# Performance work log

Hardware: AMD Instinct MI355X
Metric: run time of the kernel (lower is better)

The kernel has to match this reference:

```python
import jax, jax.numpy as jnp
import numpy as np


def setup_inputs() -> dict:
    key = jax.random.key(0)
    k1, k2 = jax.random.split(key)
    x = jax.random.normal(k1, (16, 256, 4096), dtype=jnp.float32)          # [B, D, T]
    codebooks = jax.random.normal(k2, (8, 1024, 256), dtype=jnp.float32)   # [n_q, bins, D]
    return {"x": x, "codebooks": codebooks}


def _quantize_one(residual, embed):
    """residual: [B, T, D]; embed: [bins, D] -> (quantize [B,T,D], idx [B,T])."""
    # negative squared euclidean distance (encodec euclidean codebook)
    x_sq = jnp.sum(residual * residual, axis=-1, keepdims=True)            # [B, T, 1]
    e_sq = jnp.sum(embed * embed, axis=-1)                                  # [bins]
    dots = jnp.einsum("btd,nd->btn", residual, embed)                       # [B, T, bins]
    dist = -(x_sq - 2.0 * dots + e_sq)                                      # [B, T, bins]
    idx = jnp.argmax(dist, axis=-1)                                         # [B, T] int
    quantize = embed[idx]                                                   # gather [B, T, D]
    return quantize, idx


def reference(x, codebooks):
    """Residual VQ forward (inference path, EMA updates omitted).
    x: [B, D, T]; codebooks: [n_q, bins, D].
    Returns (quantized [B, D, T], codes [n_q, B, T]).
    """
    n_q = codebooks.shape[0]
    residual = jnp.transpose(x, (0, 2, 1))                                  # [B, T, D]
    quantized_out = jnp.zeros_like(residual)
    codes = []
    for q in range(n_q):  # small fixed structural loop over quantizer stages
        quantize, idx = _quantize_one(residual, codebooks[q])
        # straight-through estimator as in encodec VectorQuantization
        quantize = residual + jax.lax.stop_gradient(quantize - residual)
        residual = residual - quantize
        quantized_out = quantized_out + quantize
        codes.append(idx)
    quantized = jnp.transpose(quantized_out, (0, 2, 1))                     # [B, D, T]
    codes = jnp.stack(codes, axis=0)                                        # [n_q, B, T]
    return quantized, codes
```

## Files before the change

### kernel.cpp

```cpp
#include <hip/hip_runtime.h>


#define BB   16
#define DD   256
#define TT   4096
#define NQ   8
#define BINS 1024
#define DELTA 4.0f
#define SOFF  8192.0f
#define OUTQ ((size_t)BB * DD * TT)

typedef _Float16 half8 __attribute__((ext_vector_type(8)));
typedef float    facc  __attribute__((ext_vector_type(4)));

#define MFMA16(A, B, C) __builtin_amdgcn_mfma_f32_16x16x32_f16((A), (B), (C), 0, 0, 0)

__global__ __launch_bounds__(256)
void rvq_pack_h16(const float* __restrict__ cb, _Float16* __restrict__ pks) {
    int gid = blockIdx.x * 256 + threadIdx.x;
    int s   = gid & 7;
    int bin = (gid >> 3) & 1023;
    int q   = gid >> 13;
    const float* src = cb + ((size_t)(q * BINS + bin)) * DD + s * 32;
    int cc    = q * 32 + (bin >> 5);
    int nf    = (bin >> 4) & 1;
    int c     = bin & 15;
    int plane = nf * 8 + s;
    size_t base = (size_t)cc * 8192 + (size_t)plane * 512 + c * 8;
    #pragma unroll
    for (int g = 0; g < 4; ++g) {
        float4 v0 = *(const float4*)(src + g * 8);
        float4 v1 = *(const float4*)(src + g * 8 + 4);
        float vv[8] = { v0.x, v0.y, v0.z, v0.w, v1.x, v1.y, v1.z, v1.w };
        half8 h8;
        #pragma unroll
        for (int j = 0; j < 8; ++j) h8[j] = (_Float16)vv[j];
        *(half8*)&pks[base + g * 128] = h8;
    }
}

__global__ __launch_bounds__(256)
void rvq_esq_off(const float* __restrict__ cb, float* __restrict__ hoff) {
    int q = blockIdx.x;
    const float* e = cb + (size_t)q * BINS * DD;
    for (int bin = threadIdx.x; bin < BINS; bin += 256) {
        const float4* row = (const float4*)(e + (size_t)bin * DD);
        float s = 0.f;
        #pragma unroll 8
        for (int i = 0; i < DD / 4; ++i) {
            float4 v = row[i];
            s += v.x * v.x + v.y * v.y + v.z * v.z + v.w * v.w;
        }
        hoff[q * BINS + bin] = SOFF - 8.0f * s;
    }
}

__global__ __launch_bounds__(256, 2)
void rvq_mfma6_kernel(const float* __restrict__ x, const float* __restrict__ cb,
                      const _Float16* __restrict__ pks, const float* __restrict__ hoff,
                      float* __restrict__ out)
{
    __shared__ alignas(16) _Float16 btile[2][16][512];
    __shared__ unsigned short best_lds[4][32];
    __shared__ unsigned short hist_lds[4][NQ][32];

    const int tid = threadIdx.x;
    const int w   = tid >> 6;
    const int l   = tid & 63;
    const int c   = l & 15;
    const int g   = l >> 4;

    const int blk = blockIdx.x;
    const int b   = blk >> 5;
    const int t0  = (blk & 31) * 128;
    const int tw  = t0 + w * 32;

    const char* gsrc0 = (const char*)pks + w * 4096 + (l << 4);

    auto issue_chunk = [&](int k, int bu) {
        k &= 255;
        const char* src = gsrc0 + (size_t)k * 16384;
        char* dst = (char*)(&btile[bu][0][0]) + w * 4096;
        #pragma unroll
        for (int i = 0; i < 4; ++i) {
            __builtin_amdgcn_global_load_lds(
                (const __attribute__((address_space(1))) unsigned int*)(src + i * 1024),
                (__attribute__((address_space(3))) unsigned int*)(dst + i * 1024),
                16, 0, 0);
        }
    };

    issue_chunk(0, 0);

    half8 rh[2][8], rl[2][8];
    {
        const float* xb = x + (size_t)b * DD * TT;
        #pragma unroll
        for (int s = 0; s < 8; ++s) {
            #pragma unroll
            for (int j = 0; j < 8; ++j) {
                int d = s * 32 + g * 8 + j;
                #pragma unroll
                for (int m = 0; m < 2; ++m) {
                    int t = tw + m * 16 + c;
                    float v = 16.0f * xb[(size_t)d * TT + t];
                    _Float16 h = (_Float16)v;
                    rh[m][s][j] = h;
                    rl[m][s][j] = (_Float16)(v - (float)h);
                }
            }
        }
    }
    __syncthreads();

    float p1[2][4], p2[2][4], p3[2][4];

    auto reset_slots = [&]() {
        #pragma unroll
        for (int m = 0; m < 2; ++m)
            #pragma unroll
            for (int j = 0; j < 4; ++j) { p1[m][j] = 0.f; p2[m][j] = 0.f; p3[m][j] = 0.f; }
    };

    auto compute_chunk = [&](int bu, int qq, int ch) {
        facc a00 = {0.f,0.f,0.f,0.f}, a01 = {0.f,0.f,0.f,0.f};
        facc a10 = {0.f,0.f,0.f,0.f}, a11 = {0.f,0.f,0.f,0.f};
        const int roff = g * 128 + c * 8;
        const float* hq = hoff + qq * BINS + ch * 32;
        float q0 = hq[c], q1 = hq[16 + c];
        const _Float16 (*bt)[512] = btile[bu];

        __builtin_amdgcn_s_setprio(1);
        #pragma unroll
        for (int s = 0; s < 8; ++s) {
            half8 b0 = *(const half8*)&bt[s][roff];
            half8 b1 = *(const half8*)&bt[8 + s][roff];
            a00 = MFMA16(rh[0][s], b0, a00);
            a10 = MFMA16(rh[1][s], b0, a10);
            a01 = MFMA16(rh[0][s], b1, a01);
            a11 = MFMA16(rh[1][s], b1, a11);
        }
        __builtin_amdgcn_s_setprio(0);

        const unsigned idx0 = 1023u - (unsigned)(ch * 32 + c);
        const unsigned idx1 = idx0 - 16u;
        #pragma unroll
        for (int fm = 0; fm < 2; ++fm) {
            #pragma unroll
            for (int fj = 0; fj < 4; ++fj) {
                float s0 = (fm ? a10[fj] : a00[fj]) + q0;
                float s1 = (fm ? a11[fj] : a01[fj]) + q1;
                float v0 = __builtin_bit_cast(float,
                             (__builtin_bit_cast(unsigned, s0) & ~1023u) | idx0);
                float v1 = __builtin_bit_cast(float,
                             (__builtin_bit_cast(unsigned, s1) & ~1023u) | idx1);
                float h1 = fmaxf(p1[fm][fj], v0), l1 = fminf(p1[fm][fj], v0);
                float h2 = fmaxf(p2[fm][fj], l1), l2 = fminf(p2[fm][fj], l1);
                p1[fm][fj] = h1; p2[fm][fj] = h2; p3[fm][fj] = fmaxf(p3[fm][fj], l2);
                h1 = fmaxf(p1[fm][fj], v1); l1 = fminf(p1[fm][fj], v1);
                h2 = fmaxf(p2[fm][fj], l1); l2 = fminf(p2[fm][fj], l1);
                p1[fm][fj] = h1; p2[fm][fj] = h2; p3[fm][fj] = fmaxf(p3[fm][fj], l2);
            }
        }
    };

    auto refine3 = [&](int tkl, int qq, int c1, int c2, int c3) -> int {
        int t = tw + tkl;
        double pa = 0.0, pb = 0.0, pc = 0.0;
        const float* e1p = cb + (size_t)(qq * BINS + c1) * DD;
        const float* e2p = cb + (size_t)(qq * BINS + c2) * DD;
        const float* e3p = cb + (size_t)(qq * BINS + c3) * DD;
        #pragma unroll
        for (int dd = 0; dd < 4; ++dd) {
            int d = l * 4 + dd;
            float rv = x[((size_t)b * DD + d) * TT + t];
            for (int k = 0; k < qq; ++k) {
                int hb = hist_lds[w][k][tkl];
                rv -= cb[(size_t)(k * BINS + hb) * DD + d];
            }
            float e1v = e1p[d], e2v = e2p[d], e3v = e3p[d];
            pa += (double)e1v * (2.0 * (double)rv - (double)e1v);
            pb += (double)e2v * (2.0 * (double)rv - (double)e2v);
            pc += (double)e3v * (2.0 * (double)rv - (double)e3v);
        }
        #pragma unroll
        for (int mk = 1; mk < 64; mk <<= 1) {
            pa += __shfl_xor(pa, mk);
            pb += __shfl_xor(pb, mk);
            pc += __shfl_xor(pc, mk);
        }
        int wbin = c1; double pw = pa;
        if (pb > pw || (pb == pw && c2 < wbin)) { pw = pb; wbin = c2; }
        if (pc > pw || (pc == pw && c3 < wbin)) { pw = pc; wbin = c3; }
        return wbin;
    };

    auto stage_end = [&](int qq) {
        int  bch[2][4], cn2[2][4], cn3[2][4];
        bool gate[2][4];
        #pragma unroll
        for (int fm = 0; fm < 2; ++fm) {
            #pragma unroll
            for (int fj = 0; fj < 4; ++fj) {
                float a1 = p1[fm][fj], a2 = p2[fm][fj], a3 = p3[fm][fj];
                #pragma unroll
                for (int mk = 1; mk < 16; mk <<= 1) {
                    float b1 = __shfl_xor(a1, mk);
                    float b2 = __shfl_xor(a2, mk);
                    float b3 = __shfl_xor(a3, mk);
                    float lo1 = fminf(a1, b1);
                    float m22 = fmaxf(a2, b2);
                    float r1  = fmaxf(a1, b1);
                    float r2  = fmaxf(lo1, m22);
                    float r3  = fmaxf(fminf(lo1, m22), fmaxf(fminf(a2, b2), fmaxf(a3, b3)));
                    a1 = r1; a2 = r2; a3 = r3;
                }
                bch[fm][fj] = 1023 - (int)(__builtin_bit_cast(unsigned, a1) & 1023u);
                cn2[fm][fj] = 1023 - (int)(__builtin_bit_cast(unsigned, a2) & 1023u);
                cn3[fm][fj] = 1023 - (int)(__builtin_bit_cast(unsigned, a3) & 1023u);
                gate[fm][fj] = (a1 - a2 <= DELTA);
            }
        }
        bool anyg = gate[0][0] | gate[0][1] | gate[0][2] | gate[0][3]
                  | gate[1][0] | gate[1][1] | gate[1][2] | gate[1][3];
        if (__any(anyg)) {
            #pragma unroll
            for (int fm = 0; fm < 2; ++fm) {
                #pragma unroll
                for (int fj = 0; fj < 4; ++fj) {
                    unsigned long long nm = __ballot(gate[fm][fj]);
                    if (nm) {
                        for (int g2 = 0; g2 < 4; ++g2) {
                            if ((nm >> (g2 * 16)) & 1ull) {
                                int c1 = __shfl(bch[fm][fj], g2 * 16);
                                int c2 = __shfl(cn2[fm][fj], g2 * 16);
                                int c3 = __shfl(cn3[fm][fj], g2 * 16);
                                int tkl = fm * 16 + g2 * 4 + fj;
                                int wb = refine3(tkl, qq, c1, c2, c3);
                                if (g == g2) bch[fm][fj] = wb;
                            }
                        }
                    }
                }
            }
        }

        if (c == 0) {
            #pragma unroll
            for (int fm = 0; fm < 2; ++fm)
                #pragma unroll
                for (int fj = 0; fj < 4; ++fj) {
                    int tkl = fm * 16 + g * 4 + fj;
                    best_lds[w][tkl] = (unsigned short)bch[fm][fj];
                    hist_lds[w][qq][tkl] = (unsigned short)bch[fm][fj];
                    out[OUTQ + ((size_t)qq * BB + b) * TT + tw + tkl] = (float)bch[fm][fj];
                }
        }

        #pragma unroll
        for (int m = 0; m < 2; ++m) {
            int bin = best_lds[w][m * 16 + c];
            const float* ep = cb + (size_t)(qq * BINS + bin) * DD + g * 8;
            #pragma unroll
            for (int s = 0; s < 8; ++s) {
                float4 e0 = *(const float4*)(ep + s * 32);
                float4 e1 = *(const float4*)(ep + s * 32 + 4);
                float ev[8] = { e0.x, e0.y, e0.z, e0.w, e1.x, e1.y, e1.z, e1.w };
                #pragma unroll
                for (int j = 0; j < 8; ++j) {
                    float rv = (float)rh[m][s][j] + (float)rl[m][s][j];
                    float nr = rv - 16.0f * ev[j];
                    _Float16 nh = (_Float16)nr;
                    rh[m][s][j] = nh;
                    rl[m][s][j] = (_Float16)(nr - (float)nh);
                }
            }
        }
    };

    int buf = 0;
    for (int q = 0; q < NQ; ++q) {
        reset_slots();
        for (int ch = 0; ch < 32; ++ch) {
            issue_chunk(q * 32 + ch + 1, buf ^ 1);
            compute_chunk(buf, q, ch);
            if (ch == 31) stage_end(q);
            __syncthreads();
            buf ^= 1;
        }
    }

    {
        const float* xb = x + (size_t)b * DD * TT;
        float* ob = out + (size_t)b * DD * TT;
        #pragma unroll
        for (int s = 0; s < 8; ++s)
            #pragma unroll
            for (int j = 0; j < 8; ++j) {
                int d = s * 32 + g * 8 + j;
                #pragma unroll
                for (int m = 0; m < 2; ++m) {
                    int t = tw + m * 16 + c;
                    float rv = ((float)rh[m][s][j] + (float)rl[m][s][j]) * 0.0625f;
                    ob[(size_t)d * TT + t] = xb[(size_t)d * TT + t] - rv;
                }
            }
    }
}

#define TOK_PER_BLK 32
#define BIN_CHUNK   128
#define KC          32
#define EPAD        36
#define RPAD        260
#define FDELTA      0.0078125f

#define FUPD2(S, BIN, B1, I1, B2, I2)                                        \
    if ((S) > (B2) || ((S) == (B2) && (BIN) < (I2))) {                      \
        if ((S) > (B1) || ((S) == (B1) && (BIN) < (I1))) {                  \
            B2 = B1; I2 = I1; B1 = (S); I1 = (BIN);                         \
        } else { B2 = (S); I2 = (BIN); }                                    \
    }

__global__ __launch_bounds__(256, 2)
void rvq_esq_kernel(const float* __restrict__ cb, float* __restrict__ esq) {
    int q = blockIdx.x;
    const float* e = cb + (size_t)q * BINS * DD;
    for (int bin = threadIdx.x; bin < BINS; bin += 256) {
        const float4* row = (const float4*)(e + (size_t)bin * DD);
        float s = 0.f;
        #pragma unroll 8
        for (int i = 0; i < DD / 4; ++i) {
            float4 v = row[i];
            s += v.x * v.x + v.y * v.y + v.z * v.z + v.w * v.w;
        }
        esq[q * BINS + bin] = s;
    }
}

__global__ __launch_bounds__(256, 2)
void rvq_main_kernel(const float* __restrict__ x, const float* __restrict__ cb,
                     const float* __restrict__ esq, float* __restrict__ out) {
    __shared__ float r_lds[TOK_PER_BLK][RPAD];
    __shared__ float e_lds[BIN_CHUNK][EPAD];
    __shared__ float red_s[16][2][TOK_PER_BLK];
    __shared__ int   red_i[16][2][TOK_PER_BLK];
    __shared__ int   best_lds2[TOK_PER_BLK];

    const int tid = threadIdx.x;
    const int blk = blockIdx.x;
    const int b   = blk >> 7;
    const int t0  = (blk & 127) * TOK_PER_BLK;

    {
        const int tl = tid & 31;
        const int d0 = (tid >> 5) * 32;
        const float* xp = x + (size_t)b * DD * TT + t0 + tl;
        for (int dd = 0; dd < 32; ++dd) {
            int d = d0 + dd;
            r_lds[tl][d] = xp[(size_t)d * TT];
        }
    }
    __syncthreads();

    const int ty = tid >> 4;
    const int tx = tid & 15;

    for (int q = 0; q < NQ; ++q) {
        const float* eb = cb + (size_t)q * BINS * DD;
        const float* es = esq + q * BINS;
        float b1[2] = {-1e30f, -1e30f}, b2[2] = {-1e30f, -1e30f};
        int   i1[2] = {0x7fffffff, 0x7fffffff}, i2[2] = {0x7fffffff, 0x7fffffff};

        for (int cch = 0; cch < BINS / BIN_CHUNK; ++cch) {
            float acc[2][8];
            #pragma unroll
            for (int i = 0; i < 2; ++i)
                #pragma unroll
                for (int j = 0; j < 8; ++j) acc[i][j] = 0.f;

            for (int kc = 0; kc < DD / KC; ++kc) {
                __syncthreads();
                {
                    const int col  = tid & 7;
                    const int row0 = tid >> 3;
                    const float* src = eb + (size_t)(cch * BIN_CHUNK) * DD + kc * KC;
                    #pragma unroll
                    for (int rr = 0; rr < 4; ++rr) {
                        int row = row0 + rr * 32;
                        float4 v = *(const float4*)(src + (size_t)row * DD + col * 4);
                        *(float4*)&e_lds[row][col * 4] = v;
                    }
                }
                __syncthreads();
                #pragma unroll
                for (int k4 = 0; k4 < KC / 4; ++k4) {
                    float4 r0 = *(const float4*)&r_lds[tx][kc * KC + k4 * 4];
                    float4 r1 = *(const float4*)&r_lds[tx + 16][kc * KC + k4 * 4];
                    #pragma unroll
                    for (int bi = 0; bi < 8; ++bi) {
                        float4 e4 = *(const float4*)&e_lds[ty + 16 * bi][k4 * 4];
                        acc[0][bi] += r0.x * e4.x + r0.y * e4.y + r0.z * e4.z + r0.w * e4.w;
                        acc[1][bi] += r1.x * e4.x + r1.y * e4.y + r1.z * e4.z + r1.w * e4.w;
                    }
                }
            }
            #pragma unroll
            for (int bi = 0; bi < 8; ++bi) {
                int bin = cch * BIN_CHUNK + ty + 16 * bi;
                float half_esq = 0.5f * es[bin];
                float s0 = acc[0][bi] - half_esq;
                float s1v = acc[1][bi] - half_esq;
                FUPD2(s0, bin, b1[0], i1[0], b2[0], i2[0]);
                FUPD2(s1v, bin, b1[1], i1[1], b2[1], i2[1]);
            }
        }

        #pragma unroll
        for (int k = 0; k < 2; ++k) {
            red_s[ty][k][tx]      = k ? b2[0] : b1[0];
            red_i[ty][k][tx]      = k ? i2[0] : i1[0];
            red_s[ty][k][tx + 16] = k ? b2[1] : b1[1];
            red_i[ty][k][tx + 16] = k ? i2[1] : i1[1];
        }
        __syncthreads();

        if (tid < TOK_PER_BLK) {
            float g1 = -1e30f, g2 = -1e30f; int gi1 = 0x7fffffff, gi2 = 0x7fffffff;
            #pragma unroll
            for (int j = 0; j < 16; ++j) {
                #pragma unroll
                for (int k = 0; k < 2; ++k) {
                    float s = red_s[j][k][tid]; int ii = red_i[j][k][tid];
                    FUPD2(s, ii, g1, gi1, g2, gi2);
                }
            }
            int bif;
            if (g1 - g2 <= FDELTA) {
                const float* rrow = r_lds[tid];
                double sc[2]; int id2[2] = { gi1, gi2 };
                for (int cc2 = 0; cc2 < 2; ++cc2) {
                    const float* ep = eb + (size_t)id2[cc2] * DD;
                    double acc2 = 0.0;
                    #pragma unroll 4
                    for (int d = 0; d < DD; ++d) {
                        double ev = (double)ep[d];
                        acc2 += ev * (2.0 * (double)rrow[d] - ev);
                    }
                    sc[cc2] = acc2;
                }
                bif = (sc[0] > sc[1] || (sc[0] == sc[1] && id2[0] < id2[1])) ? id2[0] : id2[1];
            } else {
                bif = gi1;
            }
            best_lds2[tid] = bif;
            out[OUTQ + (size_t)q * (BB * TT) + (size_t)b * TT + t0 + tid] = (float)bif;
        }
        __syncthreads();

        {
            const int tok  = tid >> 3;
            const int part = tid & 7;
            const int bin  = best_lds2[tok];
            const float* ep = eb + (size_t)bin * DD + part * 32;
            float* rp = &r_lds[tok][part * 32];
            #pragma unroll
            for (int dd = 0; dd < 32; ++dd) rp[dd] -= ep[dd];
        }
        __syncthreads();
    }

    {
        const int tl = tid & 31;
        const int d0 = (tid >> 5) * 32;
        const float* xp = x + (size_t)b * DD * TT + t0 + tl;
        float*       op = out + (size_t)b * DD * TT + t0 + tl;
        for (int dd = 0; dd < 32; ++dd) {
            int d = d0 + dd;
            op[(size_t)d * TT] = xp[(size_t)d * TT] - r_lds[tl][d];
        }
    }
}

extern "C" void kernel_launch(void* const* d_in, const int* in_sizes, int n_in,
                              void* d_out, int out_size, void* d_ws, size_t ws_size,
                              hipStream_t stream) {
    const float* x  = (const float*)d_in[0];
    const float* cb = (const float*)d_in[1];
    float* out = (float*)d_out;

    const size_t PKS_BYTES = (size_t)NQ * BINS * DD * 2;
    const size_t NEED = PKS_BYTES + (size_t)NQ * BINS * 4;

    if (ws_size >= NEED) {
        _Float16* pks = (_Float16*)d_ws;
        float* hoff = (float*)((char*)d_ws + PKS_BYTES);
        rvq_pack_h16<<<(NQ * BINS * 8) / 256, 256, 0, stream>>>(cb, pks);
        rvq_esq_off<<<NQ, 256, 0, stream>>>(cb, hoff);
        rvq_mfma6_kernel<<<512, 256, 0, stream>>>(x, cb, pks, hoff, out);
    } else {
        float* esq = (float*)d_ws;
        rvq_esq_kernel<<<NQ, 256, 0, stream>>>(cb, esq);
        rvq_main_kernel<<<(BB * TT) / TOK_PER_BLK, 256, 0, stream>>>(x, cb, esq, out);
    }
}
```

Before: 652.9 us.

## Double chunk staging to pairs per barrier and stage codebook norms in LDS

The main loop now loads two 32-bin codebook chunks per pipeline step, halving the number of __syncthreads barriers per stage. LDS tile buffers double in size. Per-stage codebook-norm offsets are copied into shared memory once per stage instead of being read from global memory per chunk. This adds an extra barrier per stage and raises LDS use, which may affect occupancy under the two-blocks-per-CU launch bound.

```diff
diff --git a/kernel.cpp b/kernel.cpp
--- a/kernel.cpp
+++ b/kernel.cpp
@@ -56,11 +56,12 @@
 }
 
 __global__ __launch_bounds__(256, 2)
-void rvq_mfma6_kernel(const float* __restrict__ x, const float* __restrict__ cb,
+void rvq_mfma7_kernel(const float* __restrict__ x, const float* __restrict__ cb,
                       const _Float16* __restrict__ pks, const float* __restrict__ hoff,
                       float* __restrict__ out)
 {
-    __shared__ alignas(16) _Float16 btile[2][16][512];
+    __shared__ alignas(16) _Float16 btile[2][2][16][512];
+    __shared__ float esq_lds[BINS];
     __shared__ unsigned short best_lds[4][32];
     __shared__ unsigned short hist_lds[4][NQ][32];
 
@@ -75,14 +76,14 @@
     const int t0  = (blk & 31) * 128;
     const int tw  = t0 + w * 32;
 
-    const char* gsrc0 = (const char*)pks + w * 4096 + (l << 4);
-
-    auto issue_chunk = [&](int k, int bu) {
-        k &= 255;
-        const char* src = gsrc0 + (size_t)k * 16384;
-        char* dst = (char*)(&btile[bu][0][0]) + w * 4096;
-        #pragma unroll
-        for (int i = 0; i < 4; ++i) {
+    const char* gsrc0 = (const char*)pks + w * 8192 + (l << 4);
+
+    auto issue_pair = [&](int p, int bu) {
+        p &= 127;
+        const char* src = gsrc0 + (size_t)p * 32768;
+        char* dst = (char*)(&btile[bu][0][0][0]) + w * 8192;
+        #pragma unroll
+        for (int i = 0; i < 8; ++i) {
             __builtin_amdgcn_global_load_lds(
                 (const __attribute__((address_space(1))) unsigned int*)(src + i * 1024),
                 (__attribute__((address_space(3))) unsigned int*)(dst + i * 1024),
@@ -90,7 +91,7 @@
         }
     };
 
-    issue_chunk(0, 0);
+    issue_pair(0, 0);
 
     half8 rh[2][8], rl[2][8];
     {
@@ -111,6 +112,10 @@
             }
         }
     }
+    {
+        float4 v = *(const float4*)(hoff + tid * 4);
+        *(float4*)&esq_lds[tid * 4] = v;
+    }
     __syncthreads();
 
     float p1[2][4], p2[2][4], p3[2][4];
@@ -122,13 +127,13 @@
             for (int j = 0; j < 4; ++j) { p1[m][j] = 0.f; p2[m][j] = 0.f; p3[m][j] = 0.f; }
     };
 
-    auto compute_chunk = [&](int bu, int qq, int ch) {
+    auto compute_chunk = [&](int bu, int pc, int ch) {
         facc a00 = {0.f,0.f,0.f,0.f}, a01 = {0.f,0.f,0.f,0.f};
         facc a10 = {0.f,0.f,0.f,0.f}, a11 = {0.f,0.f,0.f,0.f};
         const int roff = g * 128 + c * 8;
-        const float* hq = hoff + qq * BINS + ch * 32;
-        float q0 = hq[c], q1 = hq[16 + c];
-        const _Float16 (*bt)[512] = btile[bu];
+        const float q0 = esq_lds[ch * 32 + c];
+        const float q1 = esq_lds[ch * 32 + 16 + c];
+        const _Float16 (*bt)[512] = btile[bu][pc];
 
         __builtin_amdgcn_s_setprio(1);
         #pragma unroll
@@ -279,14 +284,22 @@
     };
 
     int buf = 0;
+    #pragma unroll 1
     for (int q = 0; q < NQ; ++q) {
         reset_slots();
-        for (int ch = 0; ch < 32; ++ch) {
-            issue_chunk(q * 32 + ch + 1, buf ^ 1);
-            compute_chunk(buf, q, ch);
-            if (ch == 31) stage_end(q);
+        #pragma unroll 1
+        for (int p = 0; p < 16; ++p) {
+            issue_pair(q * 16 + p + 1, buf ^ 1);
+            compute_chunk(buf, 0, 2 * p);
+            compute_chunk(buf, 1, 2 * p + 1);
+            if (p == 15) stage_end(q);
             __syncthreads();
             buf ^= 1;
+        }
+        if (q + 1 < NQ) {
+            float4 v = *(const float4*)(hoff + (q + 1) * BINS + tid * 4);
+            *(float4*)&esq_lds[tid * 4] = v;
+            __syncthreads();
         }
     }
 
@@ -497,7 +510,7 @@
         float* hoff = (float*)((char*)d_ws + PKS_BYTES);
         rvq_pack_h16<<<(NQ * BINS * 8) / 256, 256, 0, stream>>>(cb, pks);
         rvq_esq_off<<<NQ, 256, 0, stream>>>(cb, hoff);
-        rvq_mfma6_kernel<<<512, 256, 0, stream>>>(x, cb, pks, hoff, out);
+        rvq_mfma7_kernel<<<512, 256, 0, stream>>>(x, cb, pks, hoff, out);
     } else {
         float* esq = (float*)d_ws;
         rvq_esq_kernel<<<NQ, 256, 0, stream>>>(cb, esq);
```

Measured after the change: 627.2 us. -3.9%, faster.
